# Kernel tuning notes

Measured on AMD Instinct MI355X. Metric: run time of the kernel, lower is better.

The kernel has to match this reference:

```python
import jax, jax.numpy as jnp
import numpy as np

NUM_EMBEDDING = 8192
EMBEDDING_DIM = 512
BS = 16384
NEG_SLOPE = 0.01  # torch LeakyReLU default


def setup_inputs() -> dict:
    key = jax.random.key(0)
    k1, k2, k3, k4, k5, k6, k7 = jax.random.split(key, 7)
    d, K = EMBEDDING_DIM, NUM_EMBEDDING
    s1 = 1.0 / np.sqrt(d)
    return {
        "encoded_eeg": jax.random.normal(k1, (BS, d), dtype=jnp.float32),
        "encoded_mel": jax.random.normal(k2, (BS, d), dtype=jnp.float32),
        "embeddings": jax.random.normal(k3, (K, d), dtype=jnp.float32),
        "W1": jax.random.uniform(k4, (d, d), jnp.float32, -s1, s1),
        "b1": jax.random.uniform(k5, (d,), jnp.float32, -s1, s1),
        "W2": jax.random.uniform(k6, (K, d), jnp.float32, -s1, s1),
        "b2": jax.random.uniform(k7, (K,), jnp.float32, -s1, s1),
    }


def reference(encoded_eeg, encoded_mel, embeddings, W1, b1, W2, b2):
    # --- nearest-codebook indices for mel (detached in original) ---
    flat_mel = encoded_mel.reshape(-1, EMBEDDING_DIM)
    dists = (jnp.sum(embeddings ** 2, axis=1)[None, :]
             + jnp.sum(flat_mel ** 2, axis=1, keepdims=True)
             - 2.0 * flat_mel @ embeddings.T)  # [BS, K]
    mel_indices = jnp.argmin(dists, axis=-1)  # [BS]

    # --- small MLP logits over eeg ---
    flat_eeg = encoded_eeg.reshape(-1, EMBEDDING_DIM)
    h = flat_eeg @ W1.T + b1
    h = jnp.where(h >= 0, h, NEG_SLOPE * h)  # LeakyReLU
    logits = h @ W2.T + b2  # [BS, K]

    eeg_indices = jnp.argmax(logits, axis=-1)
    acc_rate = jnp.mean((eeg_indices == mel_indices).astype(jnp.float32))

    # cross entropy (mean over batch)
    logp = jax.nn.log_softmax(logits, axis=-1)
    loss = -jnp.mean(jnp.take_along_axis(logp, mel_indices[:, None], axis=1))
    return (loss, acc_rate)
```

## Files before the change

kernel.cpp:

```cpp
#include <hip/hip_runtime.h>
#include <hip/hip_bf16.h>
#include <hip/hip_fp8.h>

#define BSZ 16384
#define DIM 512
#define NEMB 8192
#define NEG 0.01f
#define NSPLIT 8
#define NG 64

typedef __attribute__((ext_vector_type(8))) short short8;
typedef __attribute__((ext_vector_type(4))) float f32x4;
typedef __attribute__((ext_vector_type(2))) long long2v;

typedef const __attribute__((address_space(1))) void GVT;
typedef __attribute__((address_space(3))) void LVT;

__device__ __forceinline__ void gl_lds16(const void* g, void* l) {
    __builtin_amdgcn_global_load_lds((GVT*)g, (LVT*)l, 16, 0, 0);
}

__device__ __forceinline__ float bf2f(unsigned short u) {
    union { unsigned int i; float f; } c; c.i = ((unsigned int)u) << 16; return c.f;
}
__device__ __forceinline__ unsigned short f2bf(float f) {
    union { __hip_bfloat16 h; unsigned short u; } c; c.h = __float2bfloat16(f); return c.u;
}
__device__ __forceinline__ unsigned char f2fp8(float f) {
    __hip_fp8_e4m3 t(f); return (unsigned char)t.__x;
}
__device__ __forceinline__ unsigned int fkey(float f) {
    unsigned int u = __float_as_uint(f);
    return u ^ ((unsigned int)((int)u >> 31) | 0x80000000u);
}

__device__ __forceinline__ size_t pack_addr(int r, int k) {
    int kg = k >> 6, ko = k & 63;
    int half = ko >> 5, lq = (ko & 31) >> 3, sub = ko & 7;
    int L = lq * 16 + (r & 15);
    return ((size_t)((r >> 4) * 8 + kg) << 10) + (size_t)(L << 4) + (half << 3) + sub;
}

__device__ __forceinline__ void pipe_barrier() {
    asm volatile("s_waitcnt vmcnt(4) lgkmcnt(0)\ns_barrier" ::: "memory");
}
__device__ __forceinline__ void plain_barrier() {
    asm volatile("s_barrier" ::: "memory");
}

#define ISSUE8(G, BUF) do { \
    int Gm = (G) & (NG - 1); \
    size_t off = (size_t)((Gm & 7) << 10); \
    size_t bo  = off + ((size_t)(Gm >> 3) << 16); \
    gl_lds16(gA8 + off,         &sA8[BUF][uWd]); \
    gl_lds16(gA8 + off + 32768, &sA8[BUF][uWd + 4096]); \
    gl_lds16(gB8 + bo,          &sB8[BUF][uWd]); \
    gl_lds16(gB8 + bo + 32768,  &sB8[BUF][uWd + 4096]); \
} while (0)

#define COMPUTE8(BUF) do { \
    long2v fa[4], fb[4]; \
    _Pragma("unroll") for (int i = 0; i < 4; i++) { \
        fa[i] = *(const long2v*)&sA8[BUF][offA[i]]; \
        fb[i] = *(const long2v*)&sB8[BUF][offB[i]]; \
    } \
    _Pragma("unroll") for (int kk = 0; kk < 2; kk++) \
        _Pragma("unroll") for (int mi = 0; mi < 4; mi++) \
            _Pragma("unroll") for (int ni = 0; ni < 4; ni++) \
                acc[mi][ni] = __builtin_amdgcn_mfma_f32_16x16x32_fp8_fp8(fa[mi][kk], fb[ni][kk], acc[mi][ni], 0, 0, 0); \
} while (0)

__global__ void k_prep(const float* __restrict__ eeg, const float* __restrict__ mel,
                       const float* __restrict__ emb, const float* __restrict__ W2,
                       const float* __restrict__ W1,
                       unsigned short* __restrict__ o_eeg, unsigned short* __restrict__ o_w1,
                       unsigned char* __restrict__ o_mel8, unsigned char* __restrict__ o_emb8,
                       unsigned char* __restrict__ o_w28,
                       float* __restrict__ enorm,
                       float* __restrict__ acc2, int* __restrict__ cnt) {
    int bid = blockIdx.x, tid = threadIdx.x;
    if (bid == 0 && tid == 0) { acc2[0] = 0.f; acc2[1] = 0.f; *cnt = 0; }
    if (bid < 1024) {
        const int n_big = BSZ * DIM / 4;
        const int n_mid = NEMB * DIM / 4;
        const int n_w1  = DIM * DIM / 4;
        const int total = n_big * 2 + n_mid * 2 + n_w1;
        for (int i = bid * 256 + tid; i < total; i += 1024 * 256) {
            int j = i;
            if (j < n_big) {
                float4 v = ((const float4*)eeg)[j];
                ushort4 o; o.x = f2bf(v.x); o.y = f2bf(v.y); o.z = f2bf(v.z); o.w = f2bf(v.w);
                ((ushort4*)o_eeg)[j] = o;
            } else if ((j -= n_big) < n_w1) {
                float4 v = ((const float4*)W1)[j];
                ushort4 o; o.x = f2bf(v.x); o.y = f2bf(v.y); o.z = f2bf(v.z); o.w = f2bf(v.w);
                ((ushort4*)o_w1)[j] = o;
            } else if ((j -= n_w1) < n_big) {
                float4 v = ((const float4*)mel)[j];
                uchar4 o; o.x = f2fp8(v.x); o.y = f2fp8(v.y); o.z = f2fp8(v.z); o.w = f2fp8(v.w);
                *(uchar4*)(o_mel8 + pack_addr(j >> 7, (j & 127) * 4)) = o;
            } else if ((j -= n_big) < n_mid) {
                float4 v = ((const float4*)emb)[j];
                uchar4 o; o.x = f2fp8(v.x); o.y = f2fp8(v.y); o.z = f2fp8(v.z); o.w = f2fp8(v.w);
                *(uchar4*)(o_emb8 + pack_addr(j >> 7, (j & 127) * 4)) = o;
            } else {
                j -= n_mid;
                float4 v = ((const float4*)W2)[j];
                uchar4 o; o.x = f2fp8(v.x); o.y = f2fp8(v.y); o.z = f2fp8(v.z); o.w = f2fp8(v.w);
                *(uchar4*)(o_w28 + pack_addr(j >> 7, (j & 127) * 4)) = o;
            }
        }
    } else {
        int w = tid >> 6, lane = tid & 63;
        int row0 = (bid - 1024) * 8 + w * 2;
        #pragma unroll
        for (int t = 0; t < 2; t++) {
            int row = row0 + t;
            const float4* p = (const float4*)(emb + (size_t)row * DIM) + lane * 2;
            float4 a = p[0], b = p[1];
            float s = a.x*a.x + a.y*a.y + a.z*a.z + a.w*a.w
                    + b.x*b.x + b.y*b.y + b.z*b.z + b.w*b.w;
            #pragma unroll
            for (int d = 1; d < 64; d <<= 1) s += __shfl_xor(s, d);
            if (lane == 0) enorm[row] = s;
        }
    }
}

__launch_bounds__(256, 2)
__global__ void k_hgemm(const unsigned short* __restrict__ A,
                        const unsigned short* __restrict__ B,
                        const float* __restrict__ b1,
                        unsigned short* __restrict__ H,
                        unsigned char* __restrict__ H8) {
    __shared__ __align__(16) unsigned short sA[4096], sB[4096];
    int tid = threadIdx.x;
    int w = tid >> 6, lane = tid & 63;
    int wr = w >> 1, wc = w & 1;
    int lquad = lane >> 4, l15 = lane & 15;
    int mt = blockIdx.x >> 2, nt = blockIdx.x & 3;
    int m0 = mt * 128, n0 = nt * 128;

    int e0 = w * 512 + lane * 8;
    int r0 = e0 >> 5, ce = e0 & 31;
    const unsigned short* gA0 = A + (m0 + r0) * DIM + ce;
    const unsigned short* gA1 = gA0 + 64 * DIM;
    const unsigned short* gB0 = B + (n0 + r0) * DIM + ce;
    const unsigned short* gB1 = gB0 + 64 * DIM;
    unsigned short* lA0 = sA + w * 512;  unsigned short* lA1 = sA + (w + 4) * 512;
    unsigned short* lB0 = sB + w * 512;  unsigned short* lB1 = sB + (w + 4) * 512;

    int offA[4], offB[4];
    #pragma unroll
    for (int i = 0; i < 4; i++) {
        offA[i] = (wr * 64 + i * 16 + l15) * 32 + lquad * 8;
        offB[i] = (wc * 64 + i * 16 + l15) * 32 + lquad * 8;
    }

    f32x4 acc[4][4];
    #pragma unroll
    for (int mi = 0; mi < 4; mi++)
        #pragma unroll
        for (int ni = 0; ni < 4; ni++) acc[mi][ni] = 0;

    for (int kk = 0; kk < 16; kk++) {
        gl_lds16(gA0, lA0); gl_lds16(gA1, lA1);
        gl_lds16(gB0, lB0); gl_lds16(gB1, lB1);
        gA0 += 32; gA1 += 32; gB0 += 32; gB1 += 32;
        __syncthreads();
        short8 af[4], bf_[4];
        #pragma unroll
        for (int i = 0; i < 4; i++) {
            af[i]  = *(const short8*)&sA[offA[i]];
            bf_[i] = *(const short8*)&sB[offB[i]];
        }
        #pragma unroll
        for (int mi = 0; mi < 4; mi++)
            #pragma unroll
            for (int ni = 0; ni < 4; ni++)
                acc[mi][ni] = __builtin_amdgcn_mfma_f32_16x16x32_bf16(af[mi], bf_[ni], acc[mi][ni], 0, 0, 0);
        __syncthreads();
    }

    #pragma unroll
    for (int ni = 0; ni < 4; ni++) {
        int col = n0 + wc * 64 + ni * 16 + l15;
        float bv = b1[col];
        #pragma unroll
        for (int mi = 0; mi < 4; mi++) {
            int rowb = m0 + wr * 64 + mi * 16 + lquad * 4;
            #pragma unroll
            for (int rg = 0; rg < 4; rg++) {
                float v = acc[mi][ni][rg] + bv;
                v = v >= 0.f ? v : NEG * v;
                H[(rowb + rg) * DIM + col] = f2bf(v);
                H8[pack_addr(rowb + rg, col)] = f2fp8(v);
            }
        }
    }
}

__launch_bounds__(256, 3)
__global__ void k_big(const unsigned char* __restrict__ Mel8,
                      const unsigned char* __restrict__ Emb8,
                      const unsigned char* __restrict__ H8,
                      const unsigned char* __restrict__ W28,
                      const float* __restrict__ enorm,
                      const float* __restrict__ b2,
                      float* __restrict__ p_s,
                      unsigned int* __restrict__ p_pmax,
                      unsigned int* __restrict__ p_pmin) {
    __shared__ __align__(16) unsigned char sA8[2][8192], sB8[2][8192];
    __shared__ float sAux[1024];
    __shared__ float red_s[256];
    __shared__ unsigned int red_pm[256];
    int tid = threadIdx.x;
    int w = tid >> 6, lane = tid & 63;
    int wr = w >> 1, wc = w & 1;
    int lquad = lane >> 4, l15 = lane & 15;
    int bid = blockIdx.x;
    int is_logits = bid & 1;
    int id = bid >> 1;
    int mt = id >> 3, split = id & 7;
    int m0 = mt * 128, nbase = split * (NEMB / NSPLIT);

    int uWd = w * 1024;
    const unsigned char* gA8 = (is_logits ? H8 : Mel8) + (size_t)(m0 + 16 * w) * 512 + lane * 16;
    const unsigned char* gB8 = (is_logits ? W28 : Emb8) + (size_t)(nbase + 16 * w) * 512 + lane * 16;

    int offA[4], offB[4];
    #pragma unroll
    for (int i = 0; i < 4; i++) {
        offA[i] = (wr * 4 + i) * 1024 + lane * 16;
        offB[i] = (wc * 4 + i) * 1024 + lane * 16;
    }

    #pragma unroll
    for (int j = 0; j < 4; j++) {
        int c = tid + j * 256;
        sAux[c] = is_logits ? b2[nbase + c] : (enorm[nbase + c] - 512.0f);
    }

    ISSUE8(0, 0);
    ISSUE8(1, 1);

    f32x4 acc[4][4];
    #pragma unroll
    for (int mi = 0; mi < 4; mi++)
        #pragma unroll
        for (int ni = 0; ni < 4; ni++) acc[mi][ni] = 0;

    float s[16];
    unsigned int pbest[16];
    unsigned int pinit = is_logits ? 0u : 0xFFFFFFFFu;
    #pragma unroll
    for (int r = 0; r < 16; r++) { s[r] = 0.f; pbest[r] = pinit; }

    for (int g = 0; g < NG; g += 2) {
        pipe_barrier();
        COMPUTE8(0);
        plain_barrier();
        ISSUE8(g + 2, 0);
        pipe_barrier();
        COMPUTE8(1);
        if (((g + 1) & 7) == 7) {
            int c0off = ((g + 1) >> 3) << 7;
            if (is_logits) {
                #pragma unroll
                for (int ni = 0; ni < 4; ni++) {
                    int j = c0off + wc * 64 + ni * 16 + l15;
                    float bb = sAux[j];
                    unsigned int ic = (unsigned int)(NEMB - 1 - (nbase + j));
                    #pragma unroll
                    for (int mi = 0; mi < 4; mi++)
                        #pragma unroll
                        for (int rg = 0; rg < 4; rg++) {
                            float logit = acc[mi][ni][rg] + bb;
                            int r = mi * 4 + rg;
                            s[r] += __expf(logit);
                            unsigned int pk = (fkey(logit) & 0xFFFFE000u) | ic;
                            pbest[r] = pbest[r] > pk ? pbest[r] : pk;
                            acc[mi][ni][rg] = 0.f;
                        }
                }
            } else {
                #pragma unroll
                for (int ni = 0; ni < 4; ni++) {
                    int j = c0off + wc * 64 + ni * 16 + l15;
                    float en = sAux[j];
                    unsigned int cl = (unsigned int)(nbase + j);
                    #pragma unroll
                    for (int mi = 0; mi < 4; mi++)
                        #pragma unroll
                        for (int rg = 0; rg < 4; rg++) {
                            float d = fmaf(-2.f, acc[mi][ni][rg], en);
                            unsigned int pk = (fkey(d) & 0xFFFFE000u) | cl;
                            int r = mi * 4 + rg;
                            pbest[r] = pbest[r] < pk ? pbest[r] : pk;
                            acc[mi][ni][rg] = 0.f;
                        }
                }
            }
        }
        plain_barrier();
        ISSUE8(g + 3, 1);
    }

    if (is_logits) {
        #pragma unroll
        for (int r = 0; r < 16; r++)
            #pragma unroll
            for (int d = 1; d < 16; d <<= 1) {
                s[r] += __shfl_xor(s[r], d);
                unsigned int o = (unsigned int)__shfl_xor((int)pbest[r], d);
                pbest[r] = pbest[r] > o ? pbest[r] : o;
            }
        if (l15 == 0) {
            #pragma unroll
            for (int mi = 0; mi < 4; mi++)
                #pragma unroll
                for (int rg = 0; rg < 4; rg++) {
                    int r2 = (wr * 64 + mi * 16 + lquad * 4 + rg) * 2 + wc;
                    red_s[r2] = s[mi * 4 + rg];
                    red_pm[r2] = pbest[mi * 4 + rg];
                }
        }
        __syncthreads();
        if (tid < 128) {
            float S = red_s[2 * tid] + red_s[2 * tid + 1];
            unsigned int a = red_pm[2 * tid], b = red_pm[2 * tid + 1];
            int pidx = split * BSZ + m0 + tid;
            p_s[pidx] = S;
            p_pmax[pidx] = a > b ? a : b;
        }
    } else {
        #pragma unroll
        for (int r = 0; r < 16; r++)
            #pragma unroll
            for (int d = 1; d < 16; d <<= 1) {
                unsigned int o = (unsigned int)__shfl_xor((int)pbest[r], d);
                pbest[r] = pbest[r] < o ? pbest[r] : o;
            }
        if (l15 == 0) {
            #pragma unroll
            for (int mi = 0; mi < 4; mi++)
                #pragma unroll
                for (int rg = 0; rg < 4; rg++)
                    red_pm[(wr * 64 + mi * 16 + lquad * 4 + rg) * 2 + wc] = pbest[mi * 4 + rg];
        }
        __syncthreads();
        if (tid < 128) {
            unsigned int a = red_pm[2 * tid], b = red_pm[2 * tid + 1];
            p_pmin[split * BSZ + m0 + tid] = a < b ? a : b;
        }
    }
}

__global__ void k_tail(const float* __restrict__ p_s, const unsigned int* __restrict__ p_pmax,
                       const unsigned int* __restrict__ p_pmin,
                       const unsigned short* __restrict__ H,
                       const float* __restrict__ W2,
                       const float* __restrict__ b2,
                       float* __restrict__ acc2, int* __restrict__ cnt,
                       float* __restrict__ out) {
    __shared__ int s_idx[256];
    __shared__ float s_l1[256], s_match[256];
    __shared__ float s_d[4];
    int bid = blockIdx.x, tid = threadIdx.x;
    int w = tid >> 6, lane = tid & 63;
    int r = bid * 256 + tid;

    float S = 0.f; unsigned int PM = 0u, PN = 0xFFFFFFFFu;
    #pragma unroll
    for (int sp = 0; sp < NSPLIT; sp++) {
        S += p_s[sp * BSZ + r];
        unsigned int a = p_pmax[sp * BSZ + r];
        PM = PM > a ? PM : a;
        unsigned int b = p_pmin[sp * BSZ + r];
        PN = PN < b ? PN : b;
    }
    int eidx = (NEMB - 1) - (int)(PM & 0x1FFFu);
    int midx = (int)(PN & 0x1FFFu);
    s_idx[tid] = midx;
    s_l1[tid] = __logf(S) - b2[midx];
    s_match[tid] = (eidx == midx) ? 1.f : 0.f;
    __syncthreads();

    float d0 = 0.f, d1 = 0.f;
    for (int j = 0; j < 64; j++) {
        int rr = w * 64 + j;
        int ridx = s_idx[rr];
        uint4 hv = *(const uint4*)(H + (size_t)(bid * 256 + rr) * DIM + lane * 8);
        const float4* wp = (const float4*)(W2 + (size_t)ridx * DIM + lane * 8);
        float4 w0 = wp[0], w1 = wp[1];
        float p = bf2f((unsigned short)(hv.x & 0xffff)) * w0.x + bf2f((unsigned short)(hv.x >> 16)) * w0.y
                + bf2f((unsigned short)(hv.y & 0xffff)) * w0.z + bf2f((unsigned short)(hv.y >> 16)) * w0.w
                + bf2f((unsigned short)(hv.z & 0xffff)) * w1.x + bf2f((unsigned short)(hv.z >> 16)) * w1.y
                + bf2f((unsigned short)(hv.w & 0xffff)) * w1.z + bf2f((unsigned short)(hv.w >> 16)) * w1.w;
        if (j & 1) d1 += p; else d0 += p;
    }
    float ds = d0 + d1;
    #pragma unroll
    for (int d = 1; d < 64; d <<= 1) ds += __shfl_xor(ds, d);
    if (lane == 0) s_d[w] = ds;

    __syncthreads();
    for (int st = 128; st > 0; st >>= 1) {
        if (tid < st) { s_l1[tid] += s_l1[tid + st]; s_match[tid] += s_match[tid + st]; }
        __syncthreads();
    }
    if (tid == 0) {
        float loss_blk = s_l1[0] - (s_d[0] + s_d[1] + s_d[2] + s_d[3]);
        atomicAdd(&acc2[0], loss_blk * (1.0f / BSZ));
        atomicAdd(&acc2[1], s_match[0] * (1.0f / BSZ));
        __threadfence();
        if (atomicAdd(cnt, 1) == 63) {
            float L = atomicAdd(&acc2[0], 0.f);
            float M = atomicAdd(&acc2[1], 0.f);
            out[0] = L; out[1] = M;
        }
    }
}

extern "C" void kernel_launch(void* const* d_in, const int* in_sizes, int n_in,
                              void* d_out, int out_size, void* d_ws, size_t ws_size,
                              hipStream_t stream) {
    const float* eeg = (const float*)d_in[0];
    const float* mel = (const float*)d_in[1];
    const float* emb = (const float*)d_in[2];
    const float* W1  = (const float*)d_in[3];
    const float* b1  = (const float*)d_in[4];
    const float* W2  = (const float*)d_in[5];
    const float* b2  = (const float*)d_in[6];
    float* out = (float*)d_out;

    unsigned short* ws_eeg = (unsigned short*)d_ws;
    unsigned short* ws_w1  = ws_eeg + (size_t)BSZ * DIM;
    unsigned short* ws_h   = ws_w1  + (size_t)DIM * DIM;
    unsigned char*  ws_h8  = (unsigned char*)(ws_h + (size_t)BSZ * DIM);
    unsigned char*  ws_mel8 = ws_h8  + (size_t)BSZ * DIM;
    unsigned char*  ws_emb8 = ws_mel8 + (size_t)BSZ * DIM;
    unsigned char*  ws_w28  = ws_emb8 + (size_t)NEMB * DIM;
    float* ws_en  = (float*)(ws_w28 + (size_t)NEMB * DIM);
    float* p_s    = ws_en + NEMB;
    unsigned int* p_pmax = (unsigned int*)(p_s + (size_t)NSPLIT * BSZ);
    unsigned int* p_pmin = p_pmax + (size_t)NSPLIT * BSZ;
    float* acc2   = (float*)(p_pmin + (size_t)NSPLIT * BSZ);
    int*   cnt    = (int*)(acc2 + 2);

    k_prep<<<2048, 256, 0, stream>>>(eeg, mel, emb, W2, W1,
                                     ws_eeg, ws_w1, ws_mel8, ws_emb8, ws_w28,
                                     ws_en, acc2, cnt);
    k_hgemm<<<(BSZ / 128) * (DIM / 128), 256, 0, stream>>>(ws_eeg, ws_w1, b1, ws_h, ws_h8);
    k_big<<<(BSZ / 128) * NSPLIT * 2, 256, 0, stream>>>(ws_mel8, ws_emb8, ws_h8, ws_w28,
                                                        ws_en, b2, p_s, p_pmax, p_pmin);
    k_tail<<<BSZ / 256, 256, 0, stream>>>(p_s, p_pmax, p_pmin, ws_h, W2, b2, acc2, cnt, out);
}
```

Measured before the change: 400.8 us.

## Use scaled 16x16x128 FP8 MFMA with a four-stage LDS pipeline

Replaces the pairs of 16x16x32 FP8 MFMAs with the gfx950 scaled 16x16x128 f8f6f4 MFMA, using unit E8M0 scales. Two consecutive K-groups are concatenated per operand, so A and B see the same K permutation and the dot product is unchanged. LDS buffers go from two to four stages, with two groups issued per iteration and one wait-plus-barrier per iteration, to cut barrier and issue overhead. The larger shared-memory footprint lowers the launch-bounds occupancy from three to two blocks per CU.

```diff
diff --git a/kernel.cpp b/kernel.cpp
--- a/kernel.cpp
+++ b/kernel.cpp
@@ -12,6 +12,8 @@
 typedef __attribute__((ext_vector_type(8))) short short8;
 typedef __attribute__((ext_vector_type(4))) float f32x4;
 typedef __attribute__((ext_vector_type(2))) long long2v;
+typedef __attribute__((ext_vector_type(4))) int i32x4;
+typedef __attribute__((ext_vector_type(8))) int i32x8;
 
 typedef const __attribute__((address_space(1))) void GVT;
 typedef __attribute__((address_space(3))) void LVT;
@@ -41,8 +43,8 @@
     return ((size_t)((r >> 4) * 8 + kg) << 10) + (size_t)(L << 4) + (half << 3) + sub;
 }
 
-__device__ __forceinline__ void pipe_barrier() {
-    asm volatile("s_waitcnt vmcnt(4) lgkmcnt(0)\ns_barrier" ::: "memory");
+__device__ __forceinline__ void pipe_barrier8() {
+    asm volatile("s_waitcnt vmcnt(8) lgkmcnt(0)\ns_barrier" ::: "memory");
 }
 __device__ __forceinline__ void plain_barrier() {
     asm volatile("s_barrier" ::: "memory");
@@ -58,16 +60,20 @@
     gl_lds16(gB8 + bo + 32768,  &sB8[BUF][uWd + 4096]); \
 } while (0)
 
-#define COMPUTE8(BUF) do { \
-    long2v fa[4], fb[4]; \
+#define COMPUTE16(BA, BB) do { \
+    i32x8 fa[4], fb[4]; \
     _Pragma("unroll") for (int i = 0; i < 4; i++) { \
-        fa[i] = *(const long2v*)&sA8[BUF][offA[i]]; \
-        fb[i] = *(const long2v*)&sB8[BUF][offB[i]]; \
+        i32x4 al = *(const i32x4*)&sA8[BA][offA[i]]; \
+        i32x4 ah = *(const i32x4*)&sA8[BB][offA[i]]; \
+        i32x4 bl = *(const i32x4*)&sB8[BA][offB[i]]; \
+        i32x4 bh = *(const i32x4*)&sB8[BB][offB[i]]; \
+        fa[i] = __builtin_shufflevector(al, ah, 0, 1, 2, 3, 4, 5, 6, 7); \
+        fb[i] = __builtin_shufflevector(bl, bh, 0, 1, 2, 3, 4, 5, 6, 7); \
     } \
-    _Pragma("unroll") for (int kk = 0; kk < 2; kk++) \
-        _Pragma("unroll") for (int mi = 0; mi < 4; mi++) \
-            _Pragma("unroll") for (int ni = 0; ni < 4; ni++) \
-                acc[mi][ni] = __builtin_amdgcn_mfma_f32_16x16x32_fp8_fp8(fa[mi][kk], fb[ni][kk], acc[mi][ni], 0, 0, 0); \
+    _Pragma("unroll") for (int mi = 0; mi < 4; mi++) \
+        _Pragma("unroll") for (int ni = 0; ni < 4; ni++) \
+            acc[mi][ni] = __builtin_amdgcn_mfma_scale_f32_16x16x128_f8f6f4( \
+                fa[mi], fb[ni], acc[mi][ni], 0, 0, 0, 0x7F7F7F7Fu, 0, 0x7F7F7F7Fu); \
 } while (0)
 
 __global__ void k_prep(const float* __restrict__ eeg, const float* __restrict__ mel,
@@ -200,7 +206,7 @@
     }
 }
 
-__launch_bounds__(256, 3)
+__launch_bounds__(256, 2)
 __global__ void k_big(const unsigned char* __restrict__ Mel8,
                       const unsigned char* __restrict__ Emb8,
                       const unsigned char* __restrict__ H8,
@@ -210,7 +216,7 @@
                       float* __restrict__ p_s,
                       unsigned int* __restrict__ p_pmax,
                       unsigned int* __restrict__ p_pmin) {
-    __shared__ __align__(16) unsigned char sA8[2][8192], sB8[2][8192];
+    __shared__ __align__(16) unsigned char sA8[4][8192], sB8[4][8192];
     __shared__ float sAux[1024];
     __shared__ float red_s[256];
     __shared__ unsigned int red_pm[256];
@@ -243,6 +249,8 @@
 
     ISSUE8(0, 0);
     ISSUE8(1, 1);
+    ISSUE8(2, 2);
+    ISSUE8(3, 3);
 
     f32x4 acc[4][4];
     #pragma unroll
@@ -257,12 +265,12 @@
     for (int r = 0; r < 16; r++) { s[r] = 0.f; pbest[r] = pinit; }
 
     for (int g = 0; g < NG; g += 2) {
-        pipe_barrier();
-        COMPUTE8(0);
+        int sa = g & 3, sb = sa + 1;
+        pipe_barrier8();
+        COMPUTE16(sa, sb);
         plain_barrier();
-        ISSUE8(g + 2, 0);
-        pipe_barrier();
-        COMPUTE8(1);
+        ISSUE8(g + 4, sa);
+        ISSUE8(g + 5, sb);
         if (((g + 1) & 7) == 7) {
             int c0off = ((g + 1) >> 3) << 7;
             if (is_logits) {
@@ -302,8 +310,6 @@
                 }
             }
         }
-        plain_barrier();
-        ISSUE8(g + 3, 1);
     }
 
     if (is_logits) {
```

New measurement: 360.3 us. 10.1% less time.
